# Kernel optimization log

Measured on AMD Instinct MI355X. Metric: run time of the kernel, lower is better.

Reference implementation:

```python
import jax, jax.numpy as jnp
import numpy as np

H = 64
IN_DIM = 32
N = 50000
E = 100000
B = 500


def setup_inputs() -> dict:
    key = jax.random.key(0)
    ks = jax.random.split(key, 16)
    def rn(k, shape, s=0.05):
        return jax.random.normal(k, shape, dtype=jnp.float32) * s
    inp = dict(
        nfeat=rn(ks[0], (N, IN_DIM), 1.0),
        efeat=rn(ks[1], (E, 5), 1.0),
        lin0_w=rn(ks[2], (IN_DIM, H)), lin0_b=jnp.zeros((H,), jnp.float32),
        ew1=rn(ks[3], (5, 128)), eb1=jnp.zeros((128,), jnp.float32),
        ew2=rn(ks[4], (128, H * H)), eb2=jnp.zeros((H * H,), jnp.float32),
        conv_b=jnp.zeros((H,), jnp.float32),
        gru_wih=rn(ks[5], (3 * H, H)), gru_whh=rn(ks[6], (3 * H, H)),
        gru_bih=jnp.zeros((3 * H,), jnp.float32), gru_bhh=jnp.zeros((3 * H,), jnp.float32),
        lstm_wih=rn(ks[7], (4 * H, 2 * H)), lstm_whh=rn(ks[8], (4 * H, H)),
        lstm_bih=jnp.zeros((4 * H,), jnp.float32), lstm_bhh=jnp.zeros((4 * H,), jnp.float32),
        fc1_w=rn(ks[9], (2 * H, H)), fc1_b=jnp.zeros((H,), jnp.float32),
        fc2_w=rn(ks[10], (H, 1)), fc2_b=jnp.zeros((1,), jnp.float32),
        src=jax.random.randint(ks[11], (E,), 0, N),
        dst=jax.random.randint(ks[12], (E,), 0, N),
        graph_id=jnp.arange(N) // (N // B),  # B graphs of equal size, sorted
        num_graphs=B,
    )
    return inp


def reference(nfeat, efeat, lin0_w, lin0_b, ew1, eb1, ew2, eb2, conv_b,
              gru_wih, gru_whh, gru_bih, gru_bhh,
              lstm_wih, lstm_whh, lstm_bih, lstm_bhh,
              fc1_w, fc1_b, fc2_w, fc2_b,
              src, dst, graph_id, num_graphs):
    n_nodes = nfeat.shape[0]
    # lin0 + relu
    h = jax.nn.relu(nfeat @ lin0_w + lin0_b)  # [N, H]
    # edge-conditioned weight matrices (same for all 3 iterations)
    We = (jax.nn.relu(efeat @ ew1 + eb1) @ ew2 + eb2).reshape(-1, H, H)  # [E, H, H]
    deg = jnp.maximum(
        jax.ops.segment_sum(jnp.ones(src.shape[0], jnp.float32), dst, num_segments=n_nodes), 1.0)
    for _ in range(3):
        # NNConv: gather src feats, per-edge matmul, scatter-mean at dst
        msg = jnp.einsum('eh,eho->eo', h[src], We)  # [E, H]
        agg = jax.ops.segment_sum(msg, dst, num_segments=n_nodes) / deg[:, None]
        m = jax.nn.relu(agg + conv_b)
        # GRU step (PyTorch gate order r,z,n)
        gi = m @ gru_wih.T + gru_bih
        gh = h @ gru_whh.T + gru_bhh
        r = jax.nn.sigmoid(gi[:, :H] + gh[:, :H])
        z = jax.nn.sigmoid(gi[:, H:2 * H] + gh[:, H:2 * H])
        n = jnp.tanh(gi[:, 2 * H:] + r * gh[:, 2 * H:])
        h = (1.0 - z) * n + z * h
    feat = h  # [N, H]
    # Set2Set pooling: 3 iters, 1-layer LSTM with input 2H
    q_star = jnp.zeros((num_graphs, 2 * H), jnp.float32)
    hh = jnp.zeros((num_graphs, H), jnp.float32)
    cc = jnp.zeros((num_graphs, H), jnp.float32)
    for _ in range(3):
        gates = q_star @ lstm_wih.T + lstm_bih + hh @ lstm_whh.T + lstm_bhh
        i = jax.nn.sigmoid(gates[:, :H])
        f = jax.nn.sigmoid(gates[:, H:2 * H])
        g = jnp.tanh(gates[:, 2 * H:3 * H])
        o = jax.nn.sigmoid(gates[:, 3 * H:])
        cc = f * cc + i * g
        hh = o * jnp.tanh(cc)
        q = hh  # [B, H]
        e = jnp.sum(feat * q[graph_id], axis=-1)  # [N]
        emax = jax.ops.segment_max(e, graph_id, num_segments=num_graphs)
        alpha = jnp.exp(e - emax[graph_id])
        denom = jax.ops.segment_sum(alpha, graph_id, num_segments=num_graphs)
        alpha = alpha / denom[graph_id]
        readout = jax.ops.segment_sum(alpha[:, None] * feat, graph_id, num_segments=num_graphs)
        q_star = jnp.concatenate([q, readout], axis=-1)  # [B, 2H]
    pred = jax.nn.relu(q_star @ fc1_w + fc1_b) @ fc2_w + fc2_b  # [B, 1]
    return pred.reshape(-1)
```

## Files before the change

kernel.cpp:

```cpp
#include <hip/hip_runtime.h>

#define HD 64
#define NNODE 50000
#define NEDGE 100000
#define NGR 500
#define NPG 100
#define EPAD 100352
#define NCH 66

typedef _Float16 f16;
typedef _Float16 f16x2 __attribute__((ext_vector_type(2)));
typedef _Float16 f16x8 __attribute__((ext_vector_type(8)));
typedef float f32x4 __attribute__((ext_vector_type(4)));

__device__ __forceinline__ float sigmoidf_(float x) { return 1.f / (1.f + __expf(-x)); }

__global__ void k_node_init(const float* __restrict__ nfeat, const float* __restrict__ w,
                            const float* __restrict__ b, float* __restrict__ h) {
    int idx = blockIdx.x * 256 + threadIdx.x;
    int n = idx >> 6, o = idx & 63;
    if (n >= NNODE) return;
    const float* nf = nfeat + n * 32;
    float acc = b[o];
#pragma unroll
    for (int i = 0; i < 32; i++) acc += nf[i] * w[i * 64 + o];
    h[idx] = fmaxf(acc, 0.f);
}

__global__ __launch_bounds__(256) void k_edge_mlp(const float* __restrict__ efeat,
                                                  const float* __restrict__ w,
                                                  const float* __restrict__ b,
                                                  f16x2* __restrict__ uP) {
    __shared__ float sef[256 * 5];
    __shared__ float sw[5 * 128];
    __shared__ float sb[128];
    int t = threadIdx.x;
    int e0 = blockIdx.x * 256;
    for (int idx = t; idx < 1280; idx += 256) {
        int gi = e0 * 5 + idx;
        sef[idx] = (gi < NEDGE * 5) ? efeat[gi] : 0.f;
    }
    for (int idx = t; idx < 640; idx += 256) sw[idx] = w[idx];
    if (t < 128) sb[t] = b[t];
    __syncthreads();
    int e = e0 + t;
    bool valid = e < NEDGE;
    float ef[5];
#pragma unroll
    for (int i = 0; i < 5; i++) ef[i] = sef[t * 5 + i];
#pragma unroll 2
    for (int c = 0; c < NCH; c++) {
        float v[2];
#pragma unroll
        for (int s = 0; s < 2; s++) {
            int kk = 2 * c + s;
            float acc = 0.f;
            if (kk < 128) {
                acc = sb[kk];
#pragma unroll
                for (int i = 0; i < 5; i++) acc += ef[i] * sw[i * 128 + kk];
                acc = fmaxf(acc, 0.f);
            } else if (kk == 128) {
                acc = 1.f;
            }
            v[s] = valid ? acc : 0.f;
        }
        f16x2 pv;
        pv[0] = (f16)v[0];
        pv[1] = (f16)v[1];
        uP[(size_t)c * EPAD + e] = pv;
    }
}

__global__ void k_pack_b(const float* __restrict__ ew2, const float* __restrict__ eb2,
                         f16* __restrict__ w2hp) {
    int idx = blockIdx.x * 256 + threadIdx.x;
    if (idx >= 540672) return;
    int q = idx & 7, l = (idx >> 3) & 63, j = (idx >> 9) & 3, s = idx >> 11;
    int k = s * 32 + (l >> 4) * 8 + q;
    int n = j * 16 + (l & 15);
    float v = 0.f;
    if (k < 8192) v = ew2[k * 64 + n];
    else if (k < 8256) v = eb2[(k - 8192) * 64 + n];
    w2hp[idx] = (f16)v;
}

__global__ void k_prep_gru2(const float* __restrict__ wih, const float* __restrict__ whh,
                            f16* __restrict__ B1, f16* __restrict__ B2) {
    int idx = blockIdx.x * 256 + threadIdx.x;
    if (idx >= 12288) return;
    int cp = idx >> 6, k = idx & 63;
    int w = cp / 48, rem = cp % 48;
    int tg = rem >> 4, cc = rem & 15;
    int orow = tg * 64 + w * 16 + cc;
    B1[idx] = (f16)wih[orow * 64 + k];
    B2[idx] = (f16)whh[orow * 64 + k];
}

__global__ void k_transpose_f32(const float* __restrict__ in, float* __restrict__ outp,
                                int rows, int cols) {
    int idx = blockIdx.x * 256 + threadIdx.x;
    if (idx >= rows * cols) return;
    int r = idx / cols, c = idx - r * cols;
    outp[c * rows + r] = in[idx];
}

__global__ void k_pad_idx(const int* __restrict__ src, const int* __restrict__ dst,
                          int* __restrict__ srcP, int* __restrict__ dstP) {
    int e = blockIdx.x * 256 + threadIdx.x;
    if (e >= EPAD) return;
    srcP[e] = (e < NEDGE) ? src[e] : 0;
    dstP[e] = (e < NEDGE) ? dst[e] : -1;
}

__global__ void k_deg_count(const int* __restrict__ dst, int* __restrict__ cnt) {
    int e = blockIdx.x * 256 + threadIdx.x;
    if (e < NEDGE) atomicAdd(&cnt[dst[e]], 1);
}
__global__ void k_deg_inv(const int* __restrict__ cnt, float* __restrict__ dinv) {
    int n = blockIdx.x * 256 + threadIdx.x;
    if (n < NNODE) dinv[n] = 1.f / (float)max(cnt[n], 1);
}

#define MSG_PHASE(BC, UC, BN, UN, CNEXT, DOPF)                                                        \
    {                                                                                                 \
        if (DOPF) {                                                                                   \
            const f16x8* gsrc = gB + (size_t)(CNEXT) * 1024 + ch * 128 + l;                           \
            _Pragma("unroll") for (int sl = 0; sl < 4; sl++) {                                        \
                BN[sl * 2] = gsrc[sl * 256];                                                          \
                BN[sl * 2 + 1] = gsrc[sl * 256 + 64];                                                 \
            }                                                                                         \
            const f16x2* us = uP + (size_t)(CNEXT) * EPAD + eb + lr;                                  \
            _Pragma("unroll") for (int i = 0; i < 8; i++) UN[i] = us[i * 16];                         \
        }                                                                                             \
        _Pragma("unroll") for (int sl = 0; sl < 4; sl++) {                                            \
            _Pragma("unroll") for (int i = 0; i < 8; i++) {                                           \
                f16x8 av = xf[i][sl & 1] * UC[i][sl >> 1];                                            \
                acc[i][0] = __builtin_amdgcn_mfma_f32_16x16x32_f16(av, BC[sl * 2], acc[i][0], 0, 0, 0);       \
                acc[i][1] = __builtin_amdgcn_mfma_f32_16x16x32_f16(av, BC[sl * 2 + 1], acc[i][1], 0, 0, 0);   \
            }                                                                                         \
        }                                                                                             \
    }

__global__ __launch_bounds__(64) void k_msg_fused(
    const float* __restrict__ h, const f16x2* __restrict__ uP, const f16* __restrict__ w2hp,
    const int* __restrict__ srcP, const int* __restrict__ dstP, float* __restrict__ agg) {
    int l = threadIdx.x;
    int wid = blockIdx.x;
    int eb = (wid >> 1) * 128;
    int ch = wid & 1;
    int lr = l & 15, lg = l >> 4;
    f16x8 xf[8][2];
#pragma unroll
    for (int i = 0; i < 8; i++) {
        const float* xb = h + (size_t)srcP[eb + i * 16 + lr] * 64;
#pragma unroll
        for (int p = 0; p < 2; p++) {
            float4 v0 = *(const float4*)(xb + p * 32 + lg * 8);
            float4 v1 = *(const float4*)(xb + p * 32 + lg * 8 + 4);
            f16x8 xv;
            xv[0] = (f16)v0.x; xv[1] = (f16)v0.y; xv[2] = (f16)v0.z; xv[3] = (f16)v0.w;
            xv[4] = (f16)v1.x; xv[5] = (f16)v1.y; xv[6] = (f16)v1.z; xv[7] = (f16)v1.w;
            xf[i][p] = xv;
        }
    }
    const f16x8* gB = (const f16x8*)w2hp;
    f32x4 acc[8][2];
#pragma unroll
    for (int i = 0; i < 8; i++) {
        acc[i][0] = (f32x4){0.f, 0.f, 0.f, 0.f};
        acc[i][1] = (f32x4){0.f, 0.f, 0.f, 0.f};
    }
    f16x8 bA[8], bB[8];
    f16x2 uA[8], uB[8];
    {
        const f16x8* gsrc = gB + ch * 128 + l;
#pragma unroll
        for (int sl = 0; sl < 4; sl++) {
            bA[sl * 2] = gsrc[sl * 256];
            bA[sl * 2 + 1] = gsrc[sl * 256 + 64];
        }
        const f16x2* us = uP + eb + lr;
#pragma unroll
        for (int i = 0; i < 8; i++) uA[i] = us[i * 16];
    }
    for (int c = 0; c < NCH; c += 2) {
        MSG_PHASE(bA, uA, bB, uB, c + 1, true);
        MSG_PHASE(bB, uB, bA, uA, c + 2, (c + 2 < NCH));
    }
#pragma unroll
    for (int i = 0; i < 8; i++) {
        int rb = eb + i * 16 + lg * 4;
        int4 d4 = *(const int4*)(dstP + rb);
#pragma unroll
        for (int r = 0; r < 4; r++) {
            int d = (r == 0) ? d4.x : (r == 1) ? d4.y : (r == 2) ? d4.z : d4.w;
            if (d >= 0) {
                float* ap = agg + (size_t)d * 64 + ch * 32 + lr;
                atomicAdd(ap, acc[i][0][r]);
                atomicAdd(ap + 16, acc[i][1][r]);
            }
        }
    }
}

#define GWP 72
__global__ __launch_bounds__(256) void k_gru2(const float* __restrict__ agg,
                                              const float* __restrict__ dinv,
                                              const float* __restrict__ convb,
                                              const f16* __restrict__ B1g,
                                              const f16* __restrict__ B2g,
                                              const float* __restrict__ bih,
                                              const float* __restrict__ bhh,
                                              float* __restrict__ h) {
    __shared__ f16 sB1[192 * GWP];
    __shared__ f16 sB2[192 * GWP];
    __shared__ f16 sM[64 * GWP];
    __shared__ f16 sH[64 * GWP];
    int t = threadIdx.x;
    int nb = blockIdx.x * 64;
    const f16x8* g1 = (const f16x8*)B1g;
    const f16x8* g2 = (const f16x8*)B2g;
#pragma unroll
    for (int it = 0; it < 6; it++) {
        int idx = t + 256 * it;
        int c = idx >> 3, k8 = idx & 7;
        *(f16x8*)(sB1 + c * GWP + k8 * 8) = g1[idx];
        *(f16x8*)(sB2 + c * GWP + k8 * 8) = g2[idx];
    }
#pragma unroll
    for (int it = 0; it < 16; it++) {
        int idx = t + 256 * it;
        int node = idx >> 6, k = idx & 63;
        int gn = nb + node;
        float mv = 0.f, hv = 0.f;
        if (gn < NNODE) {
            mv = fmaxf(agg[(size_t)gn * 64 + k] * dinv[gn] + convb[k], 0.f);
            hv = h[(size_t)gn * 64 + k];
        }
        sM[node * GWP + k] = (f16)mv;
        sH[node * GWP + k] = (f16)hv;
    }
    __syncthreads();
    int w = t >> 6, l = t & 63, lr = l & 15, lg = l >> 4;
    f32x4 aih[4][3], ahh[4][3];
#pragma unroll
    for (int i = 0; i < 4; i++)
#pragma unroll
        for (int j = 0; j < 3; j++) {
            aih[i][j] = (f32x4){0.f, 0.f, 0.f, 0.f};
            ahh[i][j] = (f32x4){0.f, 0.f, 0.f, 0.f};
        }
#pragma unroll
    for (int kk = 0; kk < 2; kk++) {
        f16x8 am[4], ah[4], b1[3], b2[3];
#pragma unroll
        for (int i = 0; i < 4; i++) {
            am[i] = *(const f16x8*)(sM + (i * 16 + lr) * GWP + kk * 32 + lg * 8);
            ah[i] = *(const f16x8*)(sH + (i * 16 + lr) * GWP + kk * 32 + lg * 8);
        }
#pragma unroll
        for (int j = 0; j < 3; j++) {
            b1[j] = *(const f16x8*)(sB1 + (w * 48 + j * 16 + lr) * GWP + kk * 32 + lg * 8);
            b2[j] = *(const f16x8*)(sB2 + (w * 48 + j * 16 + lr) * GWP + kk * 32 + lg * 8);
        }
#pragma unroll
        for (int i = 0; i < 4; i++)
#pragma unroll
            for (int j = 0; j < 3; j++) {
                aih[i][j] = __builtin_amdgcn_mfma_f32_16x16x32_f16(am[i], b1[j], aih[i][j], 0, 0, 0);
                ahh[i][j] = __builtin_amdgcn_mfma_f32_16x16x32_f16(ah[i], b2[j], ahh[i][j], 0, 0, 0);
            }
    }
    float bi0 = bih[0 * 64 + w * 16 + lr], bh0 = bhh[0 * 64 + w * 16 + lr];
    float bi1 = bih[1 * 64 + w * 16 + lr], bh1 = bhh[1 * 64 + w * 16 + lr];
    float bi2 = bih[2 * 64 + w * 16 + lr], bh2 = bhh[2 * 64 + w * 16 + lr];
#pragma unroll
    for (int i = 0; i < 4; i++)
#pragma unroll
        for (int r = 0; r < 4; r++) {
            int node = i * 16 + lg * 4 + r;
            int gn = nb + node;
            if (gn >= NNODE) continue;
            float rg = sigmoidf_(aih[i][0][r] + bi0 + ahh[i][0][r] + bh0);
            float z = sigmoidf_(aih[i][1][r] + bi1 + ahh[i][1][r] + bh1);
            float nn = tanhf(aih[i][2][r] + bi2 + rg * (ahh[i][2][r] + bh2));
            size_t off = (size_t)gn * 64 + w * 16 + lr;
            float hold = h[off];
            h[off] = (1.f - z) * nn + z * hold;
        }
}

__global__ void k_lstm(const float* __restrict__ qstar, const float* __restrict__ wihT,
                       const float* __restrict__ whhT, const float* __restrict__ bih,
                       const float* __restrict__ bhh, float* __restrict__ hhv,
                       float* __restrict__ ccv) {
    __shared__ float sq[128], sh[64], sg[256];
    int b = blockIdx.x, t = threadIdx.x;
    if (t < 128) sq[t] = qstar[b * 128 + t];
    if (t >= 128 && t < 192) sh[t - 128] = hhv[b * 64 + t - 128];
    __syncthreads();
    float g = bih[t] + bhh[t];
#pragma unroll 8
    for (int i = 0; i < 128; i++) g += sq[i] * wihT[i * 256 + t];
#pragma unroll 8
    for (int i = 0; i < 64; i++) g += sh[i] * whhT[i * 256 + t];
    sg[t] = g;
    __syncthreads();
    if (t < 64) {
        float ig = sigmoidf_(sg[t]);
        float fg = sigmoidf_(sg[64 + t]);
        float gg = tanhf(sg[128 + t]);
        float og = sigmoidf_(sg[192 + t]);
        float c = fg * ccv[b * 64 + t] + ig * gg;
        ccv[b * 64 + t] = c;
        hhv[b * 64 + t] = og * tanhf(c);
    }
}

#define FP 68
__global__ __launch_bounds__(256) void k_attn(const float* __restrict__ feat,
                                              const float* __restrict__ hhv,
                                              float* __restrict__ qstar) {
    __shared__ float sf[NPG * FP];
    __shared__ float sq[64];
    __shared__ float se[NPG];
    __shared__ float red[2];
    int g = blockIdx.x, t = threadIdx.x;
    if (t < 64) sq[t] = hhv[g * 64 + t];
    const float* fb = feat + (size_t)g * NPG * 64;
    for (int idx = t; idx < NPG * 64; idx += 256)
        sf[(idx >> 6) * FP + (idx & 63)] = fb[idx];
    __syncthreads();
    if (t < NPG) {
        float e = 0.f;
#pragma unroll 8
        for (int o = 0; o < 64; o++) e += sf[t * FP + o] * sq[o];
        se[t] = e;
    }
    __syncthreads();
    if (t < 64) {
        float m = -1e30f;
        for (int i2 = t; i2 < NPG; i2 += 64) m = fmaxf(m, se[i2]);
        for (int d = 32; d; d >>= 1) m = fmaxf(m, __shfl_down(m, d));
        if (t == 0) red[0] = m;
    }
    __syncthreads();
    float emax = red[0];
    if (t < NPG) se[t] = __expf(se[t] - emax);
    __syncthreads();
    if (t < 64) {
        float s = 0.f;
        for (int i2 = t; i2 < NPG; i2 += 64) s += se[i2];
        for (int d = 32; d; d >>= 1) s += __shfl_down(s, d);
        if (t == 0) red[1] = s;
    }
    __syncthreads();
    float dnv = 1.f / red[1];
    if (t < 64) {
        float r = 0.f;
#pragma unroll 4
        for (int n = 0; n < NPG; n++) r += se[n] * sf[n * FP + t];
        qstar[g * 128 + t] = sq[t];
        qstar[g * 128 + 64 + t] = r * dnv;
    }
}

__global__ void k_mlp(const float* __restrict__ qstar, const float* __restrict__ w1,
                      const float* __restrict__ b1, const float* __restrict__ w2,
                      const float* __restrict__ b2, float* __restrict__ out) {
    __shared__ float sq[128];
    int b = blockIdx.x, t = threadIdx.x;
    sq[t] = qstar[b * 128 + t];
    sq[64 + t] = qstar[b * 128 + 64 + t];
    __syncthreads();
    float hsum = b1[t];
#pragma unroll 8
    for (int i = 0; i < 128; i++) hsum += sq[i] * w1[i * 64 + t];
    float p = fmaxf(hsum, 0.f) * w2[t];
    for (int d = 32; d; d >>= 1) p += __shfl_down(p, d);
    if (t == 0) out[b] = p + b2[0];
}

extern "C" void kernel_launch(void* const* d_in, const int* in_sizes, int n_in,
                              void* d_out, int out_size, void* d_ws, size_t ws_size,
                              hipStream_t stream) {
    const float* nfeat = (const float*)d_in[0];
    const float* efeat = (const float*)d_in[1];
    const float* lin0_w = (const float*)d_in[2];
    const float* lin0_b = (const float*)d_in[3];
    const float* ew1 = (const float*)d_in[4];
    const float* eb1 = (const float*)d_in[5];
    const float* ew2 = (const float*)d_in[6];
    const float* eb2 = (const float*)d_in[7];
    const float* convb = (const float*)d_in[8];
    const float* gwih = (const float*)d_in[9];
    const float* gwhh = (const float*)d_in[10];
    const float* gbih = (const float*)d_in[11];
    const float* gbhh = (const float*)d_in[12];
    const float* lwih = (const float*)d_in[13];
    const float* lwhh = (const float*)d_in[14];
    const float* lbih = (const float*)d_in[15];
    const float* lbhh = (const float*)d_in[16];
    const float* fc1w = (const float*)d_in[17];
    const float* fc1b = (const float*)d_in[18];
    const float* fc2w = (const float*)d_in[19];
    const float* fc2b = (const float*)d_in[20];
    const int* src = (const int*)d_in[21];
    const int* dst = (const int*)d_in[22];
    float* out = (float*)d_out;

    char* p = (char*)d_ws;
    auto alloc = [&](size_t bytes) {
        char* q = p;
        p += (bytes + 255) & ~(size_t)255;
        return q;
    };
    f16x2* uP = (f16x2*)alloc((size_t)NCH * EPAD * 4);
    f16* w2hp = (f16*)alloc((size_t)540672 * 2);
    float* h = (float*)alloc((size_t)NNODE * 64 * 4);
    float* agg = (float*)alloc((size_t)NNODE * 64 * 4);
    int* cnt = (int*)alloc((size_t)NNODE * 4);
    float* dinv = (float*)alloc((size_t)NNODE * 4);
    float* qstar = (float*)alloc((size_t)NGR * 128 * 4);
    float* hh = (float*)alloc((size_t)NGR * 64 * 4);
    float* cc = (float*)alloc((size_t)NGR * 64 * 4);
    float* lwihT = (float*)alloc((size_t)128 * 256 * 4);
    float* lwhhT = (float*)alloc((size_t)64 * 256 * 4);
    f16* gB1 = (f16*)alloc((size_t)12288 * 2);
    f16* gB2 = (f16*)alloc((size_t)12288 * 2);
    int* srcP = (int*)alloc((size_t)EPAD * 4);
    int* dstP = (int*)alloc((size_t)EPAD * 4);
    if ((size_t)(p - (char*)d_ws) > ws_size) return;

    hipMemsetAsync(cnt, 0, (size_t)NNODE * 4, stream);
    hipMemsetAsync(qstar, 0, (size_t)NGR * 128 * 4, stream);
    hipMemsetAsync(hh, 0, (size_t)NGR * 64 * 4, stream);
    hipMemsetAsync(cc, 0, (size_t)NGR * 64 * 4, stream);

    k_node_init<<<(NNODE * 64) / 256, 256, 0, stream>>>(nfeat, lin0_w, lin0_b, h);
    k_edge_mlp<<<EPAD / 256, 256, 0, stream>>>(efeat, ew1, eb1, uP);
    k_pack_b<<<(540672 + 255) / 256, 256, 0, stream>>>(ew2, eb2, w2hp);
    k_prep_gru2<<<48, 256, 0, stream>>>(gwih, gwhh, gB1, gB2);
    k_transpose_f32<<<(256 * 128 + 255) / 256, 256, 0, stream>>>(lwih, lwihT, 256, 128);
    k_transpose_f32<<<(256 * 64 + 255) / 256, 256, 0, stream>>>(lwhh, lwhhT, 256, 64);
    k_pad_idx<<<EPAD / 256, 256, 0, stream>>>(src, dst, srcP, dstP);
    k_deg_count<<<(NEDGE + 255) / 256, 256, 0, stream>>>(dst, cnt);
    k_deg_inv<<<(NNODE + 255) / 256, 256, 0, stream>>>(cnt, dinv);

    for (int it = 0; it < 3; it++) {
        hipMemsetAsync(agg, 0, (size_t)NNODE * 64 * 4, stream);
        k_msg_fused<<<(EPAD / 128) * 2, 64, 0, stream>>>(h, uP, w2hp, srcP, dstP, agg);
        k_gru2<<<(NNODE + 63) / 64, 256, 0, stream>>>(agg, dinv, convb, gB1, gB2, gbih, gbhh, h);
    }
    for (int it = 0; it < 3; it++) {
        k_lstm<<<NGR, 256, 0, stream>>>(qstar, lwihT, lwhhT, lbih, lbhh, hh, cc);
        k_attn<<<NGR, 256, 0, stream>>>(h, hh, qstar);
    }
    k_mlp<<<NGR, 64, 0, stream>>>(qstar, fc1w, fc1b, fc2w, fc2b, out);
}
```

Before: 535.9 us.

## Switch edge message kernel to 32x32 MFMA, fuse Set2Set into one kernel, register GRU weights

The per-edge message kernel now uses 32x32x16 MFMA tiles over 64-edge blocks, with a repacked weight layout. This halves edges per wave and doubles the grid. The three LSTM/attention iterations and the final MLP are fused into a single per-graph kernel that keeps its state in shared memory, removing seven launches and three memsets. The GRU kernel loads its weight fragments straight into registers instead of staging them through shared memory. Risks are higher register pressure, and redundant weight reloads because each wave handles fewer edges.

```diff
diff --git a/kernel.cpp b/kernel.cpp
--- a/kernel.cpp
+++ b/kernel.cpp
@@ -12,6 +12,7 @@
 typedef _Float16 f16x2 __attribute__((ext_vector_type(2)));
 typedef _Float16 f16x8 __attribute__((ext_vector_type(8)));
 typedef float f32x4 __attribute__((ext_vector_type(4)));
+typedef float f32x16 __attribute__((ext_vector_type(16)));
 
 __device__ __forceinline__ float sigmoidf_(float x) { return 1.f / (1.f + __expf(-x)); }
 
@@ -76,12 +77,17 @@
                          f16* __restrict__ w2hp) {
     int idx = blockIdx.x * 256 + threadIdx.x;
     if (idx >= 540672) return;
-    int q = idx & 7, l = (idx >> 3) & 63, j = (idx >> 9) & 3, s = idx >> 11;
-    int k = s * 32 + (l >> 4) * 8 + q;
-    int n = j * 16 + (l & 15);
+    int q = idx & 7;
+    int F = idx >> 3;
+    int l = F & 63;
+    int ks = (F >> 6) & 7;
+    int ch = (F >> 9) & 1;
+    int c = F >> 10;
+    int kg = c * 128 + ks * 16 + (l >> 5) * 8 + q;
+    int n = ch * 32 + (l & 31);
     float v = 0.f;
-    if (k < 8192) v = ew2[k * 64 + n];
-    else if (k < 8256) v = eb2[(k - 8192) * 64 + n];
+    if (kg < 8192) v = ew2[kg * 64 + n];
+    else if (kg < 8256) v = eb2[(kg - 8192) * 64 + n];
     w2hp[idx] = (f16)v;
 }
 
@@ -122,83 +128,64 @@
     if (n < NNODE) dinv[n] = 1.f / (float)max(cnt[n], 1);
 }
 
-#define MSG_PHASE(BC, UC, BN, UN, CNEXT, DOPF)                                                        \
-    {                                                                                                 \
-        if (DOPF) {                                                                                   \
-            const f16x8* gsrc = gB + (size_t)(CNEXT) * 1024 + ch * 128 + l;                           \
-            _Pragma("unroll") for (int sl = 0; sl < 4; sl++) {                                        \
-                BN[sl * 2] = gsrc[sl * 256];                                                          \
-                BN[sl * 2 + 1] = gsrc[sl * 256 + 64];                                                 \
-            }                                                                                         \
-            const f16x2* us = uP + (size_t)(CNEXT) * EPAD + eb + lr;                                  \
-            _Pragma("unroll") for (int i = 0; i < 8; i++) UN[i] = us[i * 16];                         \
-        }                                                                                             \
-        _Pragma("unroll") for (int sl = 0; sl < 4; sl++) {                                            \
-            _Pragma("unroll") for (int i = 0; i < 8; i++) {                                           \
-                f16x8 av = xf[i][sl & 1] * UC[i][sl >> 1];                                            \
-                acc[i][0] = __builtin_amdgcn_mfma_f32_16x16x32_f16(av, BC[sl * 2], acc[i][0], 0, 0, 0);       \
-                acc[i][1] = __builtin_amdgcn_mfma_f32_16x16x32_f16(av, BC[sl * 2 + 1], acc[i][1], 0, 0, 0);   \
-            }                                                                                         \
-        }                                                                                             \
-    }
-
 __global__ __launch_bounds__(64) void k_msg_fused(
     const float* __restrict__ h, const f16x2* __restrict__ uP, const f16* __restrict__ w2hp,
     const int* __restrict__ srcP, const int* __restrict__ dstP, float* __restrict__ agg) {
     int l = threadIdx.x;
     int wid = blockIdx.x;
-    int eb = (wid >> 1) * 128;
+    int eb = (wid >> 1) * 64;
     int ch = wid & 1;
-    int lr = l & 15, lg = l >> 4;
-    f16x8 xf[8][2];
-#pragma unroll
-    for (int i = 0; i < 8; i++) {
-        const float* xb = h + (size_t)srcP[eb + i * 16 + lr] * 64;
-#pragma unroll
-        for (int p = 0; p < 2; p++) {
-            float4 v0 = *(const float4*)(xb + p * 32 + lg * 8);
-            float4 v1 = *(const float4*)(xb + p * 32 + lg * 8 + 4);
+    int lm = l & 31, hi = l >> 5;
+    f16x8 xf[2][4];
+#pragma unroll
+    for (int i = 0; i < 2; i++) {
+        const float* xb = h + (size_t)srcP[eb + i * 32 + lm] * 64;
+#pragma unroll
+        for (int h4 = 0; h4 < 4; h4++) {
+            float4 v0 = *(const float4*)(xb + h4 * 16 + hi * 8);
+            float4 v1 = *(const float4*)(xb + h4 * 16 + hi * 8 + 4);
             f16x8 xv;
             xv[0] = (f16)v0.x; xv[1] = (f16)v0.y; xv[2] = (f16)v0.z; xv[3] = (f16)v0.w;
             xv[4] = (f16)v1.x; xv[5] = (f16)v1.y; xv[6] = (f16)v1.z; xv[7] = (f16)v1.w;
-            xf[i][p] = xv;
-        }
-    }
-    const f16x8* gB = (const f16x8*)w2hp;
-    f32x4 acc[8][2];
-#pragma unroll
-    for (int i = 0; i < 8; i++) {
-        acc[i][0] = (f32x4){0.f, 0.f, 0.f, 0.f};
-        acc[i][1] = (f32x4){0.f, 0.f, 0.f, 0.f};
-    }
-    f16x8 bA[8], bB[8];
-    f16x2 uA[8], uB[8];
-    {
-        const f16x8* gsrc = gB + ch * 128 + l;
-#pragma unroll
-        for (int sl = 0; sl < 4; sl++) {
-            bA[sl * 2] = gsrc[sl * 256];
-            bA[sl * 2 + 1] = gsrc[sl * 256 + 64];
-        }
-        const f16x2* us = uP + eb + lr;
-#pragma unroll
-        for (int i = 0; i < 8; i++) uA[i] = us[i * 16];
-    }
-    for (int c = 0; c < NCH; c += 2) {
-        MSG_PHASE(bA, uA, bB, uB, c + 1, true);
-        MSG_PHASE(bB, uB, bA, uA, c + 2, (c + 2 < NCH));
-    }
-#pragma unroll
-    for (int i = 0; i < 8; i++) {
-        int rb = eb + i * 16 + lg * 4;
-        int4 d4 = *(const int4*)(dstP + rb);
-#pragma unroll
-        for (int r = 0; r < 4; r++) {
-            int d = (r == 0) ? d4.x : (r == 1) ? d4.y : (r == 2) ? d4.z : d4.w;
-            if (d >= 0) {
-                float* ap = agg + (size_t)d * 64 + ch * 32 + lr;
-                atomicAdd(ap, acc[i][0][r]);
-                atomicAdd(ap + 16, acc[i][1][r]);
+            xf[i][h4] = xv;
+        }
+    }
+    const f16x8* gBp = (const f16x8*)w2hp + ch * 512 + l;
+    const f16x2* up0 = uP + eb + lm;
+    const f16x2* up1 = up0 + 32;
+    f32x16 acc0, acc1;
+#pragma unroll
+    for (int r = 0; r < 16; r++) { acc0[r] = 0.f; acc1[r] = 0.f; }
+    f16x2 uA0 = up0[0], uA1 = up1[0];
+    up0 += EPAD; up1 += EPAD;
+    for (int c = 0; c < NCH; c++) {
+        const f16x8* bb = gBp + (size_t)c * 1024;
+        f16x8 bf[8];
+#pragma unroll
+        for (int ks = 0; ks < 8; ks++) bf[ks] = bb[ks * 64];
+        f16x2 uB0, uB1;
+        if (c + 1 < NCH) { uB0 = up0[0]; uB1 = up1[0]; up0 += EPAD; up1 += EPAD; }
+#pragma unroll
+        for (int ks = 0; ks < 8; ks++) {
+            f16 u0 = uA0[ks >> 2], u1 = uA1[ks >> 2];
+            f16x8 av0 = xf[0][ks & 3] * u0;
+            f16x8 av1 = xf[1][ks & 3] * u1;
+            acc0 = __builtin_amdgcn_mfma_f32_32x32x16_f16(av0, bf[ks], acc0, 0, 0, 0);
+            acc1 = __builtin_amdgcn_mfma_f32_32x32x16_f16(av1, bf[ks], acc1, 0, 0, 0);
+        }
+        uA0 = uB0; uA1 = uB1;
+    }
+#pragma unroll
+    for (int i = 0; i < 2; i++) {
+        int rbase = eb + i * 32 + 4 * hi;
+#pragma unroll
+        for (int b = 0; b < 4; b++) {
+            int4 d4 = *(const int4*)(dstP + rbase + 8 * b);
+#pragma unroll
+            for (int rr = 0; rr < 4; rr++) {
+                int d = (rr == 0) ? d4.x : (rr == 1) ? d4.y : (rr == 2) ? d4.z : d4.w;
+                float v = (i == 0) ? acc0[b * 4 + rr] : acc1[b * 4 + rr];
+                if (d >= 0) atomicAdd(agg + (size_t)d * 64 + ch * 32 + lm, v);
             }
         }
     }
@@ -213,21 +200,20 @@
                                               const float* __restrict__ bih,
                                               const float* __restrict__ bhh,
                                               float* __restrict__ h) {
-    __shared__ f16 sB1[192 * GWP];
-    __shared__ f16 sB2[192 * GWP];
     __shared__ f16 sM[64 * GWP];
     __shared__ f16 sH[64 * GWP];
     int t = threadIdx.x;
     int nb = blockIdx.x * 64;
-    const f16x8* g1 = (const f16x8*)B1g;
-    const f16x8* g2 = (const f16x8*)B2g;
-#pragma unroll
-    for (int it = 0; it < 6; it++) {
-        int idx = t + 256 * it;
-        int c = idx >> 3, k8 = idx & 7;
-        *(f16x8*)(sB1 + c * GWP + k8 * 8) = g1[idx];
-        *(f16x8*)(sB2 + c * GWP + k8 * 8) = g2[idx];
-    }
+    int w = t >> 6, l = t & 63, lr = l & 15, lg = l >> 4;
+    f16x8 b1[2][3], b2[2][3];
+#pragma unroll
+    for (int kk = 0; kk < 2; kk++)
+#pragma unroll
+        for (int j = 0; j < 3; j++) {
+            size_t off = (size_t)(w * 48 + j * 16 + lr) * 64 + kk * 32 + lg * 8;
+            b1[kk][j] = *(const f16x8*)(B1g + off);
+            b2[kk][j] = *(const f16x8*)(B2g + off);
+        }
 #pragma unroll
     for (int it = 0; it < 16; it++) {
         int idx = t + 256 * it;
@@ -242,7 +228,6 @@
         sH[node * GWP + k] = (f16)hv;
     }
     __syncthreads();
-    int w = t >> 6, l = t & 63, lr = l & 15, lg = l >> 4;
     f32x4 aih[4][3], ahh[4][3];
 #pragma unroll
     for (int i = 0; i < 4; i++)
@@ -253,23 +238,18 @@
         }
 #pragma unroll
     for (int kk = 0; kk < 2; kk++) {
-        f16x8 am[4], ah[4], b1[3], b2[3];
+        f16x8 am[4], ah[4];
 #pragma unroll
         for (int i = 0; i < 4; i++) {
             am[i] = *(const f16x8*)(sM + (i * 16 + lr) * GWP + kk * 32 + lg * 8);
             ah[i] = *(const f16x8*)(sH + (i * 16 + lr) * GWP + kk * 32 + lg * 8);
         }
 #pragma unroll
-        for (int j = 0; j < 3; j++) {
-            b1[j] = *(const f16x8*)(sB1 + (w * 48 + j * 16 + lr) * GWP + kk * 32 + lg * 8);
-            b2[j] = *(const f16x8*)(sB2 + (w * 48 + j * 16 + lr) * GWP + kk * 32 + lg * 8);
-        }
-#pragma unroll
         for (int i = 0; i < 4; i++)
 #pragma unroll
             for (int j = 0; j < 3; j++) {
-                aih[i][j] = __builtin_amdgcn_mfma_f32_16x16x32_f16(am[i], b1[j], aih[i][j], 0, 0, 0);
-                ahh[i][j] = __builtin_amdgcn_mfma_f32_16x16x32_f16(ah[i], b2[j], ahh[i][j], 0, 0, 0);
+                aih[i][j] = __builtin_amdgcn_mfma_f32_16x16x32_f16(am[i], b1[kk][j], aih[i][j], 0, 0, 0);
+                ahh[i][j] = __builtin_amdgcn_mfma_f32_16x16x32_f16(ah[i], b2[kk][j], ahh[i][j], 0, 0, 0);
             }
     }
     float bi0 = bih[0 * 64 + w * 16 + lr], bh0 = bhh[0 * 64 + w * 16 + lr];
@@ -291,95 +271,91 @@
         }
 }
 
-__global__ void k_lstm(const float* __restrict__ qstar, const float* __restrict__ wihT,
-                       const float* __restrict__ whhT, const float* __restrict__ bih,
-                       const float* __restrict__ bhh, float* __restrict__ hhv,
-                       float* __restrict__ ccv) {
-    __shared__ float sq[128], sh[64], sg[256];
-    int b = blockIdx.x, t = threadIdx.x;
-    if (t < 128) sq[t] = qstar[b * 128 + t];
-    if (t >= 128 && t < 192) sh[t - 128] = hhv[b * 64 + t - 128];
-    __syncthreads();
-    float g = bih[t] + bhh[t];
-#pragma unroll 8
-    for (int i = 0; i < 128; i++) g += sq[i] * wihT[i * 256 + t];
-#pragma unroll 8
-    for (int i = 0; i < 64; i++) g += sh[i] * whhT[i * 256 + t];
-    sg[t] = g;
-    __syncthreads();
-    if (t < 64) {
-        float ig = sigmoidf_(sg[t]);
-        float fg = sigmoidf_(sg[64 + t]);
-        float gg = tanhf(sg[128 + t]);
-        float og = sigmoidf_(sg[192 + t]);
-        float c = fg * ccv[b * 64 + t] + ig * gg;
-        ccv[b * 64 + t] = c;
-        hhv[b * 64 + t] = og * tanhf(c);
-    }
-}
-
 #define FP 68
-__global__ __launch_bounds__(256) void k_attn(const float* __restrict__ feat,
-                                              const float* __restrict__ hhv,
-                                              float* __restrict__ qstar) {
+__global__ __launch_bounds__(256) void k_s2s(const float* __restrict__ feat,
+                                             const float* __restrict__ wihT,
+                                             const float* __restrict__ whhT,
+                                             const float* __restrict__ lbih,
+                                             const float* __restrict__ lbhh,
+                                             const float* __restrict__ fc1w,
+                                             const float* __restrict__ fc1b,
+                                             const float* __restrict__ fc2w,
+                                             const float* __restrict__ fc2b,
+                                             float* __restrict__ out) {
     __shared__ float sf[NPG * FP];
-    __shared__ float sq[64];
+    __shared__ float sq[128];
+    __shared__ float sh[64], scc[64];
+    __shared__ float sg[256];
     __shared__ float se[NPG];
     __shared__ float red[2];
     int g = blockIdx.x, t = threadIdx.x;
-    if (t < 64) sq[t] = hhv[g * 64 + t];
     const float* fb = feat + (size_t)g * NPG * 64;
     for (int idx = t; idx < NPG * 64; idx += 256)
         sf[(idx >> 6) * FP + (idx & 63)] = fb[idx];
+    if (t < 128) sq[t] = 0.f;
+    if (t >= 128 && t < 192) { sh[t - 128] = 0.f; scc[t - 128] = 0.f; }
     __syncthreads();
-    if (t < NPG) {
-        float e = 0.f;
+    for (int it = 0; it < 3; it++) {
+        float gate = lbih[t] + lbhh[t];
 #pragma unroll 8
-        for (int o = 0; o < 64; o++) e += sf[t * FP + o] * sq[o];
-        se[t] = e;
-    }
-    __syncthreads();
+        for (int i = 0; i < 128; i++) gate += sq[i] * wihT[i * 256 + t];
+#pragma unroll 8
+        for (int i = 0; i < 64; i++) gate += sh[i] * whhT[i * 256 + t];
+        sg[t] = gate;
+        __syncthreads();
+        if (t < 64) {
+            float ig = sigmoidf_(sg[t]);
+            float fg = sigmoidf_(sg[64 + t]);
+            float gg = tanhf(sg[128 + t]);
+            float og = sigmoidf_(sg[192 + t]);
+            float c = fg * scc[t] + ig * gg;
+            scc[t] = c;
+            float hv = og * tanhf(c);
+            sh[t] = hv;
+            sq[t] = hv;
+        }
+        __syncthreads();
+        if (t < NPG) {
+            float e = 0.f;
+#pragma unroll 8
+            for (int o = 0; o < 64; o++) e += sf[t * FP + o] * sh[o];
+            se[t] = e;
+        }
+        __syncthreads();
+        if (t < 64) {
+            float m = -1e30f;
+            for (int i2 = t; i2 < NPG; i2 += 64) m = fmaxf(m, se[i2]);
+            for (int d = 32; d; d >>= 1) m = fmaxf(m, __shfl_down(m, d));
+            if (t == 0) red[0] = m;
+        }
+        __syncthreads();
+        float emax = red[0];
+        if (t < NPG) se[t] = __expf(se[t] - emax);
+        __syncthreads();
+        if (t < 64) {
+            float s = 0.f;
+            for (int i2 = t; i2 < NPG; i2 += 64) s += se[i2];
+            for (int d = 32; d; d >>= 1) s += __shfl_down(s, d);
+            if (t == 0) red[1] = s;
+        }
+        __syncthreads();
+        if (t < 64) {
+            float dnv = 1.f / red[1];
+            float r = 0.f;
+#pragma unroll 4
+            for (int n = 0; n < NPG; n++) r += se[n] * sf[n * FP + t];
+            sq[64 + t] = r * dnv;
+        }
+        __syncthreads();
+    }
     if (t < 64) {
-        float m = -1e30f;
-        for (int i2 = t; i2 < NPG; i2 += 64) m = fmaxf(m, se[i2]);
-        for (int d = 32; d; d >>= 1) m = fmaxf(m, __shfl_down(m, d));
-        if (t == 0) red[0] = m;
-    }
-    __syncthreads();
-    float emax = red[0];
-    if (t < NPG) se[t] = __expf(se[t] - emax);
-    __syncthreads();
-    if (t < 64) {
-        float s = 0.f;
-        for (int i2 = t; i2 < NPG; i2 += 64) s += se[i2];
-        for (int d = 32; d; d >>= 1) s += __shfl_down(s, d);
-        if (t == 0) red[1] = s;
-    }
-    __syncthreads();
-    float dnv = 1.f / red[1];
-    if (t < 64) {
-        float r = 0.f;
-#pragma unroll 4
-        for (int n = 0; n < NPG; n++) r += se[n] * sf[n * FP + t];
-        qstar[g * 128 + t] = sq[t];
-        qstar[g * 128 + 64 + t] = r * dnv;
-    }
-}
-
-__global__ void k_mlp(const float* __restrict__ qstar, const float* __restrict__ w1,
-                      const float* __restrict__ b1, const float* __restrict__ w2,
-                      const float* __restrict__ b2, float* __restrict__ out) {
-    __shared__ float sq[128];
-    int b = blockIdx.x, t = threadIdx.x;
-    sq[t] = qstar[b * 128 + t];
-    sq[64 + t] = qstar[b * 128 + 64 + t];
-    __syncthreads();
-    float hsum = b1[t];
+        float hsum = fc1b[t];
 #pragma unroll 8
-    for (int i = 0; i < 128; i++) hsum += sq[i] * w1[i * 64 + t];
-    float p = fmaxf(hsum, 0.f) * w2[t];
-    for (int d = 32; d; d >>= 1) p += __shfl_down(p, d);
-    if (t == 0) out[b] = p + b2[0];
+        for (int i = 0; i < 128; i++) hsum += sq[i] * fc1w[i * 64 + t];
+        float p = fmaxf(hsum, 0.f) * fc2w[t];
+        for (int d = 32; d; d >>= 1) p += __shfl_down(p, d);
+        if (t == 0) out[g] = p + fc2b[0];
+    }
 }
 
 extern "C" void kernel_launch(void* const* d_in, const int* in_sizes, int n_in,
@@ -422,9 +398,6 @@
     float* agg = (float*)alloc((size_t)NNODE * 64 * 4);
     int* cnt = (int*)alloc((size_t)NNODE * 4);
     float* dinv = (float*)alloc((size_t)NNODE * 4);
-    float* qstar = (float*)alloc((size_t)NGR * 128 * 4);
-    float* hh = (float*)alloc((size_t)NGR * 64 * 4);
-    float* cc = (float*)alloc((size_t)NGR * 64 * 4);
     float* lwihT = (float*)alloc((size_t)128 * 256 * 4);
     float* lwhhT = (float*)alloc((size_t)64 * 256 * 4);
     f16* gB1 = (f16*)alloc((size_t)12288 * 2);
@@ -434,9 +407,6 @@
     if ((size_t)(p - (char*)d_ws) > ws_size) return;
 
     hipMemsetAsync(cnt, 0, (size_t)NNODE * 4, stream);
-    hipMemsetAsync(qstar, 0, (size_t)NGR * 128 * 4, stream);
-    hipMemsetAsync(hh, 0, (size_t)NGR * 64 * 4, stream);
-    hipMemsetAsync(cc, 0, (size_t)NGR * 64 * 4, stream);
 
     k_node_init<<<(NNODE * 64) / 256, 256, 0, stream>>>(nfeat, lin0_w, lin0_b, h);
     k_edge_mlp<<<EPAD / 256, 256, 0, stream>>>(efeat, ew1, eb1, uP);
@@ -450,12 +420,8 @@
 
     for (int it = 0; it < 3; it++) {
         hipMemsetAsync(agg, 0, (size_t)NNODE * 64 * 4, stream);
-        k_msg_fused<<<(EPAD / 128) * 2, 64, 0, stream>>>(h, uP, w2hp, srcP, dstP, agg);
+        k_msg_fused<<<(EPAD / 64) * 2, 64, 0, stream>>>(h, uP, w2hp, srcP, dstP, agg);
         k_gru2<<<(NNODE + 63) / 64, 256, 0, stream>>>(agg, dinv, convb, gB1, gB2, gbih, gbhh, h);
     }
-    for (int it = 0; it < 3; it++) {
-        k_lstm<<<NGR, 256, 0, stream>>>(qstar, lwihT, lwhhT, lbih, lbhh, hh, cc);
-        k_attn<<<NGR, 256, 0, stream>>>(h, hh, qstar);
-    }
-    k_mlp<<<NGR, 64, 0, stream>>>(qstar, fc1w, fc1b, fc2w, fc2b, out);
-}
+    k_s2s<<<NGR, 256, 0, stream>>>(h, lwihT, lwhhT, lbih, lbhh, fc1w, fc1b, fc2w, fc2b, out);
+}
```

Measured after the change: 634.2 us. 18.4% more time.
